# Kernel tuning notes

Measured on AMD Instinct MI355X. Metric: run time of the kernel, lower is better.

Reference implementation:

```python
import jax, jax.numpy as jnp
import numpy as np

B, S, D, H = 8, 1025, 768, 12
HD = D // H  # 64

def setup_inputs() -> dict:
    key = jax.random.key(0)
    ks = jax.random.split(key, 5)
    scale = 0.02
    return {
        "hidden_states": jax.random.normal(ks[0], (B, S, D), jnp.float32),
        "rel_bias": jax.random.normal(ks[1], (1, H, S, S), jnp.float32),
        "Wq": jax.random.normal(ks[2], (D, D), jnp.float32) * scale,
        "bq": jnp.zeros((D,), jnp.float32),
        "Wk": jax.random.normal(ks[3], (D, D), jnp.float32) * scale,
        "bk": jnp.zeros((D,), jnp.float32),
        "Wv": jax.random.normal(ks[4], (D, D), jnp.float32) * scale,
        "bv": jnp.zeros((D,), jnp.float32),
    }

def reference(hidden_states, rel_bias, Wq, bq, Wk, bk, Wv, bv):
    b, s, d = hidden_states.shape
    def split_heads(t):  # [B,S,D] -> [B,H,S,hd]
        return t.reshape(b, s, H, HD).transpose(0, 2, 1, 3)
    q = split_heads(hidden_states @ Wq + bq)
    k = split_heads(hidden_states @ Wk + bk)
    v = split_heads(hidden_states @ Wv + bv)
    inv_sqrt_hd = 1.0 / jnp.sqrt(jnp.asarray(HD, q.dtype))
    scores = jnp.einsum("bhqd,bhkd->bhqk", q, k) * inv_sqrt_hd
    scores = scores + rel_bias  # broadcast [1,H,S,S]
    probs = jax.nn.softmax(scores, axis=-1)
    ctx = jnp.einsum("bhqk,bhkd->bhqd", probs, v)
    out = ctx.transpose(0, 2, 1, 3).reshape(b, s, d)
    return out
```

## Files before the change

kernel.cpp:

```cpp
#include <hip/hip_runtime.h>

using f32x4  = __attribute__((ext_vector_type(4))) float;
using bf16x8 = __attribute__((ext_vector_type(8))) short;

#define SEQ 1025
#define NH  12

__device__ __forceinline__ unsigned short f2bf(float f) {
  unsigned u = __float_as_uint(f);
  u += 0x7FFFu + ((u >> 16) & 1u);
  return (unsigned short)(u >> 16);
}

__device__ __forceinline__ unsigned short f2bf_p(float f) {
  return (unsigned short)((__float_as_uint(f) + 0x8000u) >> 16);
}

__device__ __forceinline__ void async16(const void* g, void* s) {
  __builtin_amdgcn_global_load_lds(
      (const __attribute__((address_space(1))) void*)g,
      (__attribute__((address_space(3))) void*)s, 16, 0, 0);
}

__global__ __launch_bounds__(256) void conv_x(const float* __restrict__ X,
                                              ushort* __restrict__ Xb) {
  int t = blockIdx.x * 256 + threadIdx.x;
  if (t >= 8320 * 96) return;
  int row = t / 96;
  size_t e = (size_t)t * 8;
  union { uint4 q; ushort us[8]; } o;
  if (row < 8200) {
    float4 f0 = *(const float4*)(X + e);
    float4 f1 = *(const float4*)(X + e + 4);
    o.us[0] = f2bf(f0.x); o.us[1] = f2bf(f0.y); o.us[2] = f2bf(f0.z); o.us[3] = f2bf(f0.w);
    o.us[4] = f2bf(f1.x); o.us[5] = f2bf(f1.y); o.us[6] = f2bf(f1.z); o.us[7] = f2bf(f1.w);
  } else {
    o.q = make_uint4(0, 0, 0, 0);
  }
  *(uint4*)(Xb + e) = o.q;
}

__global__ __launch_bounds__(256) void pack_w(const float* __restrict__ Wq,
                                              const float* __restrict__ Wk,
                                              const float* __restrict__ Wv,
                                              ushort* __restrict__ Wt,
                                              const float* __restrict__ bq,
                                              const float* __restrict__ bk,
                                              const float* __restrict__ bv,
                                              float* __restrict__ bc) {
  if (blockIdx.y == 0 && blockIdx.x < 9) {
    int t2 = blockIdx.x * 256 + threadIdx.x;
    if (t2 < 768) bc[t2] = bq[t2];
    else if (t2 < 1536) bc[t2] = bk[t2 - 768];
    else if (t2 < 2304) bc[t2] = bv[t2 - 1536];
  }
  __shared__ float tile[32][33];
  const int nt = blockIdx.x;
  const int kt = blockIdx.y;
  const int sel = nt / 24;
  const int o0 = (nt - sel * 24) * 32;
  const int k0 = kt * 32;
  const float* W = sel == 0 ? Wq : sel == 1 ? Wk : Wv;
  const int t = threadIdx.x;
  const int x = t & 31, y = t >> 5;
  for (int p = 0; p < 4; ++p)
    tile[y + p * 8][x] = W[(size_t)(k0 + y + p * 8) * 768 + o0 + x];
  __syncthreads();
  for (int p = 0; p < 4; ++p) {
    const int nl = y + p * 8;
    Wt[(size_t)(nt * 32 + nl) * 768 + k0 + x] = f2bf(tile[x][nl]);
  }
}

__global__ __launch_bounds__(256, 4) void repack_bias_frag(
    const float* __restrict__ rel, float* __restrict__ bf) {
  __shared__ float lds[16][580];
  const int id = blockIdx.x;
  const int half = id & 1;
  const int hw = id >> 1;
  const int h = hw / 72, w = hw - h * 72;
  const int t = threadIdx.x;
  const int W = half ? 512 : 576;
  const int cbase = half * 576;
  const float* src = rel + (size_t)h * SEQ * SEQ;
  for (int r = 0; r < 16; ++r) {
    int q = w * 16 + r; if (q > 1024) q = 1024;
    const float* row = src + (size_t)q * SEQ;
    for (int c = t; c < W; c += 256) {
      int col = cbase + c;
      lds[r][c] = (col <= 1024) ? row[col] * 1.44269504f : -3.0e30f;
    }
  }
  __syncthreads();
  const int lane = t >> 2, ct = t & 3;
  const int l16 = lane & 15, quad = lane >> 4;
  const int nkt = half ? 8 : 9;
  for (int ktl = 0; ktl < nkt; ++ktl) {
    const int kt = half * 9 + ktl;
    const int col = ktl * 64 + ct * 16 + l16;
    f32x4 v;
    v[0] = lds[quad * 4 + 0][col];
    v[1] = lds[quad * 4 + 1][col];
    v[2] = lds[quad * 4 + 2][col];
    v[3] = lds[quad * 4 + 3][col];
    *(f32x4*)(bf + (((size_t)h * 17 + kt) * 72 + w) * 1024 + lane * 16 + ct * 4) = v;
  }
}

__global__ __launch_bounds__(256) void gemm_qkv(const ushort* __restrict__ A,
                                                const ushort* __restrict__ Bt,
                                                const float* __restrict__ bias,
                                                ushort* __restrict__ Qo,
                                                ushort* __restrict__ Ko,
                                                ushort* __restrict__ Vo) {
  __shared__ ushort a_sm[128 * 32];
  __shared__ ushort b_sm[128 * 32];
  __shared__ ushort c_sm[64 * 136];
  const int t = threadIdx.x;
  const int lane = t & 63, wave = t >> 6;
  const int quad = lane >> 4, l16 = lane & 15;
  const int wrow = wave >> 1, wcol = wave & 1;
  const int m0 = blockIdx.x * 128, n0 = blockIdx.y * 128;

  f32x4 acc[4][4] = {};

  const ushort* a_g = A + (size_t)m0 * 768;
  const ushort* b_g = Bt + (size_t)n0 * 768;

  for (int k0 = 0; k0 < 768; k0 += 32) {
    __syncthreads();
    for (int r = 0; r < 2; ++r) {
      int c = r * 256 + t;
      int row = c >> 2;
      int colb = (c & 3) * 16;
      async16((const char*)(a_g + (size_t)row * 768 + k0) + colb, (char*)a_sm + c * 16);
      async16((const char*)(b_g + (size_t)row * 768 + k0) + colb, (char*)b_sm + c * 16);
    }
    __syncthreads();
    bf16x8 af[4], bfr[4];
    for (int i = 0; i < 4; ++i) {
      af[i]  = *(const bf16x8*)(a_sm + (wrow * 64 + i * 16 + l16) * 32 + quad * 8);
      bfr[i] = *(const bf16x8*)(b_sm + (wcol * 64 + i * 16 + l16) * 32 + quad * 8);
    }
    for (int i = 0; i < 4; ++i)
      for (int j = 0; j < 4; ++j)
        acc[i][j] = __builtin_amdgcn_mfma_f32_16x16x32_bf16(af[i], bfr[j], acc[i][j], 0, 0, 0);
  }

  const int sel = n0 / 768;
  const int o0 = n0 - sel * 768;
  const int hh0 = o0 >> 6;
  ushort* dst = sel == 0 ? Qo : sel == 1 ? Ko : Vo;
  float bvj[4];
  for (int j = 0; j < 4; ++j) bvj[j] = bias[n0 + wcol * 64 + j * 16 + l16];

  for (int p = 0; p < 2; ++p) {
    __syncthreads();
    if (wrow == p) {
      for (int i = 0; i < 4; ++i)
        for (int j = 0; j < 4; ++j)
          for (int r = 0; r < 4; ++r)
            c_sm[(i * 16 + quad * 4 + r) * 136 + wcol * 64 + j * 16 + l16] =
                f2bf(acc[i][j][r] + bvj[j]);
    }
    __syncthreads();
    const int head = t >> 7;
    const int ci = t & 127;
    for (int k = 0; k < 4; ++k) {
      int ch = ci + 128 * k;
      int row = ch >> 3, off = (ch & 7) * 8;
      int gm = m0 + p * 64 + row;
      if (gm < 8200) {
        int bb = gm / 1025, ss = gm - bb * 1025;
        uint4 v = *(const uint4*)(c_sm + row * 136 + head * 64 + off);
        *(uint4*)(dst + (((size_t)(bb * NH + hh0 + head) * SEQ + ss) << 6) + off) = v;
      }
    }
  }
}

__global__ __launch_bounds__(256, 4) void attn(const ushort* __restrict__ Qb,
                                               const ushort* __restrict__ Kb,
                                               const ushort* __restrict__ Vb,
                                               const float* __restrict__ biasF,
                                               float* __restrict__ out) {
  __shared__ char smem[36864];
  ushort* p_sm = (ushort*)smem;
  ushort* k_sm = (ushort*)(smem + 18432);
  ushort* v_sm = (ushort*)(smem + 27648);

  const int t = threadIdx.x;
  const int lane = t & 63, wave = t >> 6;
  const int quad = lane >> 4, l16 = lane & 15;

  const int id = blockIdx.x;
  const int x = id & 7, s = id >> 3;
  const int Gg = s / 9, qt = s - Gg * 9;
  const int G = Gg * 8 + x;
  const int b = G / 12, h = G - b * 12;
  const int q0 = qt * 128;

  const size_t bh = (size_t)(b * NH + h) * SEQ * 64;
  const ushort* Qp = Qb + bh;
  const ushort* Kp = Kb + bh;
  const ushort* Vp = Vb + bh;

  uint4 kpre0, kpre1, vpre0, vpre1;
  const int vkp2 = t & 31, vhb = (t >> 5) * 8;

  auto issue_kv = [&](int kb) {
    {
      int c = t, row = c >> 3, cb = (c & 7) * 8;
      int rk = kb + row; if (rk > 1024) rk = 1024;
      kpre0 = *(const uint4*)(Kp + (size_t)rk * 64 + cb);
    }
    {
      int c = t + 256, row = c >> 3, cb = (c & 7) * 8;
      int rk = kb + row; if (rk > 1024) rk = 1024;
      kpre1 = *(const uint4*)(Kp + (size_t)rk * 64 + cb);
    }
    {
      int r0 = kb + vkp2 * 2;
      int r0c = r0 > 1024 ? 1024 : r0;
      int r1c = r0 + 1 > 1024 ? 1024 : r0 + 1;
      vpre0 = *(const uint4*)(Vp + (size_t)r0c * 64 + vhb);
      vpre1 = *(const uint4*)(Vp + (size_t)r1c * 64 + vhb);
    }
  };

  issue_kv(0);

  ushort* pw = p_sm + wave * (32 * 72);
  const int qbase = q0 + wave * 32;
  for (int i = 0; i < 4; ++i) {
    int c = lane + 64 * i;
    int row = c >> 3, cb = (c & 7) * 8;
    int rq = qbase + row; if (rq > 1024) rq = 1024;
    *(uint4*)(pw + row * 72 + cb) = *(const uint4*)(Qp + (size_t)rq * 64 + cb);
  }
  bf16x8 qf[2][2];
  for (int rt = 0; rt < 2; ++rt)
    for (int ks = 0; ks < 2; ++ks)
      qf[rt][ks] = *(const bf16x8*)(pw + (rt * 16 + l16) * 72 + ks * 32 + quad * 8);

  float lst[8] = {0, 0, 0, 0, 0, 0, 0, 0};
  f32x4 oacc[2][4] = {};
  const float c_scale = 0.18033688f;
  const float* bf_base = biasF +
      ((size_t)h * 17 * 72 + (qt * 8 + wave * 2)) * 1024 + (lane << 4);

  for (int kt = 0; kt < 17; ++kt) {
    __syncthreads();
    {
      int c = t;
      *(uint4*)(k_sm + (c >> 3) * 72 + (c & 7) * 8) = kpre0;
      c = t + 256;
      *(uint4*)(k_sm + (c >> 3) * 72 + (c & 7) * 8) = kpre1;
    }
    {
      union { uint4 q; ushort us[8]; } e0, e1;
      e0.q = vpre0; e1.q = vpre1;
      for (int e = 0; e < 8; ++e)
        *(unsigned*)(v_sm + (vhb + e) * 72 + vkp2 * 2) =
            (unsigned)e0.us[e] | ((unsigned)e1.us[e] << 16);
    }
    __syncthreads();

    const float* bfp = bf_base + (size_t)kt * (72 * 1024);
    f32x4 br[2][4];
    for (int rt = 0; rt < 2; ++rt)
      for (int ct = 0; ct < 4; ++ct)
        br[rt][ct] = *(const f32x4*)(bfp + rt * 1024 + ct * 4);

    if (kt < 16) issue_kv(kt * 64 + 64);

    f32x4 sc[2][4] = {};
    for (int ct = 0; ct < 4; ++ct)
      for (int ks = 0; ks < 2; ++ks) {
        bf16x8 kf = *(const bf16x8*)(k_sm + (ct * 16 + l16) * 72 + ks * 32 + quad * 8);
        sc[0][ct] = __builtin_amdgcn_mfma_f32_16x16x32_bf16(qf[0][ks], kf, sc[0][ct], 0, 0, 0);
        sc[1][ct] = __builtin_amdgcn_mfma_f32_16x16x32_bf16(qf[1][ks], kf, sc[1][ct], 0, 0, 0);
      }

    for (int rt = 0; rt < 2; ++rt)
      for (int ct = 0; ct < 4; ++ct)
        for (int r2 = 0; r2 < 4; ++r2) {
          float p = __builtin_amdgcn_exp2f(
              fmaf(sc[rt][ct][r2], c_scale, br[rt][ct][r2]));
          lst[rt * 4 + r2] += p;
          pw[(rt * 16 + quad * 4 + r2) * 72 + ct * 16 + l16] = f2bf_p(p);
        }

    for (int ks = 0; ks < 2; ++ks) {
      bf16x8 pf0 = *(const bf16x8*)(pw + l16 * 72 + ks * 32 + quad * 8);
      bf16x8 pf1 = *(const bf16x8*)(pw + (16 + l16) * 72 + ks * 32 + quad * 8);
      for (int c4 = 0; c4 < 4; ++c4) {
        bf16x8 vf = *(const bf16x8*)(v_sm + (c4 * 16 + l16) * 72 + ks * 32 + quad * 8);
        oacc[0][c4] = __builtin_amdgcn_mfma_f32_16x16x32_bf16(pf0, vf, oacc[0][c4], 0, 0, 0);
        oacc[1][c4] = __builtin_amdgcn_mfma_f32_16x16x32_bf16(pf1, vf, oacc[1][c4], 0, 0, 0);
      }
    }
  }

  for (int si = 0; si < 8; ++si) {
    float s2 = lst[si];
    s2 += __shfl_xor(s2, 1);
    s2 += __shfl_xor(s2, 2);
    s2 += __shfl_xor(s2, 4);
    s2 += __shfl_xor(s2, 8);
    lst[si] = s2;
  }
  for (int rt = 0; rt < 2; ++rt)
    for (int r2 = 0; r2 < 4; ++r2) {
      int sr = qbase + rt * 16 + quad * 4 + r2;
      if (sr < SEQ) {
        float inv = 1.0f / lst[rt * 4 + r2];
        float* op = out + ((size_t)b * SEQ + sr) * 768 + h * 64;
        for (int c4 = 0; c4 < 4; ++c4)
          op[c4 * 16 + l16] = oacc[rt][c4][r2] * inv;
      }
    }
}

extern "C" void kernel_launch(void* const* d_in, const int* in_sizes, int n_in,
                              void* d_out, int out_size, void* d_ws, size_t ws_size,
                              hipStream_t stream) {
  const float* X  = (const float*)d_in[0];
  const float* rb = (const float*)d_in[1];
  const float* Wq = (const float*)d_in[2];
  const float* bq = (const float*)d_in[3];
  const float* Wk = (const float*)d_in[4];
  const float* bk = (const float*)d_in[5];
  const float* Wv = (const float*)d_in[6];
  const float* bv = (const float*)d_in[7];
  float* out = (float*)d_out;
  char* ws = (char*)d_ws;

  ushort* Qb    = (ushort*)ws;
  ushort* Kb    = (ushort*)(ws + 12595200);
  ushort* Vb    = (ushort*)(ws + 25190400);
  ushort* Xb    = (ushort*)(ws + 37785600);
  ushort* Wt    = (ushort*)(ws + 50565120);
  float*  biasc = (float*)(ws + 54104064);
  float*  biasF = (float*)(ws + 37785600);

  conv_x<<<3120, 256, 0, stream>>>(X, Xb);
  pack_w<<<dim3(72, 24), 256, 0, stream>>>(Wq, Wk, Wv, Wt, bq, bk, bv, biasc);
  gemm_qkv<<<dim3(65, 18), 256, 0, stream>>>(Xb, Wt, biasc, Qb, Kb, Vb);
  repack_bias_frag<<<NH * 72 * 2, 256, 0, stream>>>(rb, biasF);
  attn<<<864, 256, 0, stream>>>(Qb, Kb, Vb, biasF, out);
}
```

Baseline: 317.8 us.

## Merge prep and GEMM/bias-repack launches into combined grids; prefetch bias tiles in attention

Folds conv_x and pack_w into one launch. When the workspace is large enough, the QKV GEMM and the relative-bias repack also run in a single launch, using a separate workspace region so they no longer alias. This cuts launch count and lets the independent GEMM and repack blocks share the device at once. In attention, the next key tile's bias fragment is loaded one iteration ahead to hide global-load latency. The trade-off is more registers and higher shared-memory use for the fused kernel.

Result: slower. 400.5 us (+26.0%).

```diff
diff --git a/kernel.cpp b/kernel.cpp
--- a/kernel.cpp
+++ b/kernel.cpp
@@ -22,9 +22,10 @@
       (__attribute__((address_space(3))) void*)s, 16, 0, 0);
 }
 
-__global__ __launch_bounds__(256) void conv_x(const float* __restrict__ X,
-                                              ushort* __restrict__ Xb) {
-  int t = blockIdx.x * 256 + threadIdx.x;
+
+__device__ __forceinline__ void conv_x_body(int bx, const float* __restrict__ X,
+                                            ushort* __restrict__ Xb) {
+  int t = bx * 256 + threadIdx.x;
   if (t >= 8320 * 96) return;
   int row = t / 96;
   size_t e = (size_t)t * 8;
@@ -40,23 +41,23 @@
   *(uint4*)(Xb + e) = o.q;
 }
 
-__global__ __launch_bounds__(256) void pack_w(const float* __restrict__ Wq,
-                                              const float* __restrict__ Wk,
-                                              const float* __restrict__ Wv,
-                                              ushort* __restrict__ Wt,
-                                              const float* __restrict__ bq,
-                                              const float* __restrict__ bk,
-                                              const float* __restrict__ bv,
-                                              float* __restrict__ bc) {
-  if (blockIdx.y == 0 && blockIdx.x < 9) {
-    int t2 = blockIdx.x * 256 + threadIdx.x;
+__device__ __forceinline__ void pack_w_body(int j, const float* __restrict__ Wq,
+                                            const float* __restrict__ Wk,
+                                            const float* __restrict__ Wv,
+                                            ushort* __restrict__ Wt,
+                                            const float* __restrict__ bq,
+                                            const float* __restrict__ bk,
+                                            const float* __restrict__ bv,
+                                            float* __restrict__ bc,
+                                            float (*tile)[33]) {
+  const int nt = j % 72;
+  const int kt = j / 72;
+  if (kt == 0 && nt < 9) {
+    int t2 = nt * 256 + threadIdx.x;
     if (t2 < 768) bc[t2] = bq[t2];
     else if (t2 < 1536) bc[t2] = bk[t2 - 768];
     else if (t2 < 2304) bc[t2] = bv[t2 - 1536];
   }
-  __shared__ float tile[32][33];
-  const int nt = blockIdx.x;
-  const int kt = blockIdx.y;
   const int sel = nt / 24;
   const int o0 = (nt - sel * 24) * 32;
   const int k0 = kt * 32;
@@ -72,10 +73,9 @@
   }
 }
 
-__global__ __launch_bounds__(256, 4) void repack_bias_frag(
-    const float* __restrict__ rel, float* __restrict__ bf) {
-  __shared__ float lds[16][580];
-  const int id = blockIdx.x;
+__device__ __forceinline__ void repack_body(int id, const float* __restrict__ rel,
+                                            float* __restrict__ bf,
+                                            float (*lds)[580]) {
   const int half = id & 1;
   const int hw = id >> 1;
   const int h = hw / 72, w = hw - h * 72;
@@ -107,20 +107,22 @@
   }
 }
 
-__global__ __launch_bounds__(256) void gemm_qkv(const ushort* __restrict__ A,
-                                                const ushort* __restrict__ Bt,
-                                                const float* __restrict__ bias,
-                                                ushort* __restrict__ Qo,
-                                                ushort* __restrict__ Ko,
-                                                ushort* __restrict__ Vo) {
-  __shared__ ushort a_sm[128 * 32];
-  __shared__ ushort b_sm[128 * 32];
-  __shared__ ushort c_sm[64 * 136];
+__device__ __forceinline__ void gemm_body(int mb, int nb,
+                                          const ushort* __restrict__ A,
+                                          const ushort* __restrict__ Bt,
+                                          const float* __restrict__ bias,
+                                          ushort* __restrict__ Qo,
+                                          ushort* __restrict__ Ko,
+                                          ushort* __restrict__ Vo,
+                                          char* smem) {
+  ushort* a_sm = (ushort*)smem;
+  ushort* b_sm = (ushort*)(smem + 8192);
+  ushort* c_sm = (ushort*)(smem + 16384);
   const int t = threadIdx.x;
   const int lane = t & 63, wave = t >> 6;
   const int quad = lane >> 4, l16 = lane & 15;
   const int wrow = wave >> 1, wcol = wave & 1;
-  const int m0 = blockIdx.x * 128, n0 = blockIdx.y * 128;
+  const int m0 = mb * 128, n0 = nb * 128;
 
   f32x4 acc[4][4] = {};
 
@@ -179,12 +181,56 @@
   }
 }
 
+
+__global__ __launch_bounds__(256) void prep(const float* __restrict__ X,
+                                            ushort* __restrict__ Xb,
+                                            const float* __restrict__ Wq,
+                                            const float* __restrict__ Wk,
+                                            const float* __restrict__ Wv,
+                                            ushort* __restrict__ Wt,
+                                            const float* __restrict__ bq,
+                                            const float* __restrict__ bk,
+                                            const float* __restrict__ bv,
+                                            float* __restrict__ bc) {
+  __shared__ __align__(16) float tile[32][33];
+  const int bx = blockIdx.x;
+  if (bx < 3120) conv_x_body(bx, X, Xb);
+  else pack_w_body(bx - 3120, Wq, Wk, Wv, Wt, bq, bk, bv, bc, tile);
+}
+
+__global__ __launch_bounds__(256, 4) void gemm_repack(
+    const ushort* __restrict__ A, const ushort* __restrict__ Bt,
+    const float* __restrict__ biasc, ushort* __restrict__ Qo,
+    ushort* __restrict__ Ko, ushort* __restrict__ Vo,
+    const float* __restrict__ rel, float* __restrict__ bf) {
+  __shared__ __align__(16) char smem[37120];
+  const int bx = blockIdx.x;
+  if (bx < 1170) gemm_body(bx % 65, bx / 65, A, Bt, biasc, Qo, Ko, Vo, smem);
+  else repack_body(bx - 1170, rel, bf, (float(*)[580])smem);
+}
+
+__global__ __launch_bounds__(256) void gemm_qkv_k(const ushort* __restrict__ A,
+                                                  const ushort* __restrict__ Bt,
+                                                  const float* __restrict__ biasc,
+                                                  ushort* __restrict__ Qo,
+                                                  ushort* __restrict__ Ko,
+                                                  ushort* __restrict__ Vo) {
+  __shared__ __align__(16) char smem[33792];
+  gemm_body(blockIdx.x, blockIdx.y, A, Bt, biasc, Qo, Ko, Vo, smem);
+}
+
+__global__ __launch_bounds__(256, 4) void repack_k(const float* __restrict__ rel,
+                                                   float* __restrict__ bf) {
+  __shared__ __align__(16) float lds[16][580];
+  repack_body(blockIdx.x, rel, bf, lds);
+}
+
 __global__ __launch_bounds__(256, 4) void attn(const ushort* __restrict__ Qb,
                                                const ushort* __restrict__ Kb,
                                                const ushort* __restrict__ Vb,
                                                const float* __restrict__ biasF,
                                                float* __restrict__ out) {
-  __shared__ char smem[36864];
+  __shared__ __align__(16) char smem[36864];
   ushort* p_sm = (ushort*)smem;
   ushort* k_sm = (ushort*)(smem + 18432);
   ushort* v_sm = (ushort*)(smem + 27648);
@@ -228,7 +274,14 @@
     }
   };
 
+  const float* bf_base = biasF +
+      ((size_t)h * 17 * 72 + (qt * 8 + wave * 2)) * 1024 + (lane << 4);
+
   issue_kv(0);
+  f32x4 brp[2][4];
+  for (int rt = 0; rt < 2; ++rt)
+    for (int ct = 0; ct < 4; ++ct)
+      brp[rt][ct] = *(const f32x4*)(bf_base + rt * 1024 + ct * 4);
 
   ushort* pw = p_sm + wave * (32 * 72);
   const int qbase = q0 + wave * 32;
@@ -246,8 +299,6 @@
   float lst[8] = {0, 0, 0, 0, 0, 0, 0, 0};
   f32x4 oacc[2][4] = {};
   const float c_scale = 0.18033688f;
-  const float* bf_base = biasF +
-      ((size_t)h * 17 * 72 + (qt * 8 + wave * 2)) * 1024 + (lane << 4);
 
   for (int kt = 0; kt < 17; ++kt) {
     __syncthreads();
@@ -265,12 +316,6 @@
             (unsigned)e0.us[e] | ((unsigned)e1.us[e] << 16);
     }
     __syncthreads();
-
-    const float* bfp = bf_base + (size_t)kt * (72 * 1024);
-    f32x4 br[2][4];
-    for (int rt = 0; rt < 2; ++rt)
-      for (int ct = 0; ct < 4; ++ct)
-        br[rt][ct] = *(const f32x4*)(bfp + rt * 1024 + ct * 4);
 
     if (kt < 16) issue_kv(kt * 64 + 64);
 
@@ -286,10 +331,17 @@
       for (int ct = 0; ct < 4; ++ct)
         for (int r2 = 0; r2 < 4; ++r2) {
           float p = __builtin_amdgcn_exp2f(
-              fmaf(sc[rt][ct][r2], c_scale, br[rt][ct][r2]));
+              fmaf(sc[rt][ct][r2], c_scale, brp[rt][ct][r2]));
           lst[rt * 4 + r2] += p;
           pw[(rt * 16 + quad * 4 + r2) * 72 + ct * 16 + l16] = f2bf_p(p);
         }
+
+    if (kt < 16) {
+      const float* bfp = bf_base + (size_t)(kt + 1) * (72 * 1024);
+      for (int rt = 0; rt < 2; ++rt)
+        for (int ct = 0; ct < 4; ++ct)
+          brp[rt][ct] = *(const f32x4*)(bfp + rt * 1024 + ct * 4);
+    }
 
     for (int ks = 0; ks < 2; ++ks) {
       bf16x8 pf0 = *(const bf16x8*)(pw + l16 * 72 + ks * 32 + quad * 8);
@@ -342,11 +394,16 @@
   ushort* Xb    = (ushort*)(ws + 37785600);
   ushort* Wt    = (ushort*)(ws + 50565120);
   float*  biasc = (float*)(ws + 54104064);
-  float*  biasF = (float*)(ws + 37785600);
-
-  conv_x<<<3120, 256, 0, stream>>>(X, Xb);
-  pack_w<<<dim3(72, 24), 256, 0, stream>>>(Wq, Wk, Wv, Wt, bq, bk, bv, biasc);
-  gemm_qkv<<<dim3(65, 18), 256, 0, stream>>>(Xb, Wt, biasc, Qb, Kb, Vb);
-  repack_bias_frag<<<NH * 72 * 2, 256, 0, stream>>>(rb, biasF);
+
+  const bool bigws = ws_size >= 114275328ULL;
+  float* biasF = bigws ? (float*)(ws + 54113280) : (float*)(ws + 37785600);
+
+  prep<<<3120 + 1728, 256, 0, stream>>>(X, Xb, Wq, Wk, Wv, Wt, bq, bk, bv, biasc);
+  if (bigws) {
+    gemm_repack<<<1170 + 1728, 256, 0, stream>>>(Xb, Wt, biasc, Qb, Kb, Vb, rb, biasF);
+  } else {
+    gemm_qkv_k<<<dim3(65, 18), 256, 0, stream>>>(Xb, Wt, biasc, Qb, Kb, Vb);
+    repack_k<<<NH * 72 * 2, 256, 0, stream>>>(rb, biasF);
+  }
   attn<<<864, 256, 0, stream>>>(Qb, Kb, Vb, biasF, out);
 }
```
